# Kernel tuning notes

Hardware: AMD Instinct MI355X
Metric: run time of the kernel (lower is better)

## Reference

```python
import jax, jax.numpy as jnp
import numpy as np

B, LI, LC = 2, 1024, 256
H, NH, HD = 1024, 16, 64
MLP = 4096
EPS = 1e-6


def rmsnorm(x, w):
    return x * jax.lax.rsqrt(jnp.mean(x * x, axis=-1, keepdims=True) + EPS) * w


def apply_rope(x, cos, sin):
    # x: [B, NH, S, HD]; cos/sin: [S, HD]; rotate-half convention
    x1, x2 = jnp.split(x, 2, axis=-1)
    rot = jnp.concatenate([-x2, x1], axis=-1)
    return x * cos + rot * sin


def project_qkv(x, w, b):
    # x: [B, S, H] -> q,k,v each [B, NH, S, HD]
    bsz, s, _ = x.shape
    qkv = (x @ w.T + b).reshape(bsz, s, 3, NH, HD)
    qkv = jnp.transpose(qkv, (2, 0, 3, 1, 4))
    return qkv[0], qkv[1], qkv[2]


def setup_inputs() -> dict:
    key = jax.random.key(0)
    ks = iter(jax.random.split(key, 40))
    n = lambda shape, scale=1.0: jax.random.normal(next(ks), shape, dtype=jnp.float32) * scale
    xav = lambda fo, fi: n((fo, fi), float(np.sqrt(2.0 / (fo + fi))))
    inp = {
        'image_tokens': n((B, LI, H)),
        'condition_tokens': n((B, LC, H)),
        'image_rope_cos': n((LI, HD)),
        'image_rope_sin': n((LI, HD)),
        'cond_rope_cos': n((LC, HD)),
        'cond_rope_sin': n((LC, HD)),
        'img_norm1_w': jnp.ones((H,)), 'cond_norm1_w': jnp.ones((H,)),
        'img_qkv_w': xav(3 * H, H), 'img_qkv_b': jnp.zeros((3 * H,)),
        'cond_qkv_w': xav(3 * H, H), 'cond_qkv_b': jnp.zeros((3 * H,)),
        'img_qn_w': jnp.ones((HD,)), 'img_kn_w': jnp.ones((HD,)),
        'cond_qn_w': jnp.ones((HD,)), 'cond_kn_w': jnp.ones((HD,)),
        'img_out_w': xav(H, H), 'img_out_b': jnp.zeros((H,)),
        'cond_out_w': xav(H, H), 'cond_out_b': jnp.zeros((H,)),
        'img_norm2_w': jnp.ones((H,)), 'cond_norm2_w': jnp.ones((H,)),
        'img_mlp_w1': xav(MLP, H), 'img_mlp_b1': jnp.zeros((MLP,)),
        'img_mlp_w2': xav(MLP, H), 'img_mlp_b2': jnp.zeros((MLP,)),
        'img_mlp_w3': xav(H, MLP), 'img_mlp_b3': jnp.zeros((H,)),
        'cond_mlp_w1': xav(MLP, H), 'cond_mlp_b1': jnp.zeros((MLP,)),
        'cond_mlp_w2': xav(MLP, H), 'cond_mlp_b2': jnp.zeros((MLP,)),
        'cond_mlp_w3': xav(H, MLP), 'cond_mlp_b3': jnp.zeros((H,)),
        'alpha': jnp.zeros((1,)), 'beta': jnp.zeros((1,)),
    }
    return inp


def swiglu(x, w1, b1, w2, b2, w3, b3):
    return (jax.nn.silu(x @ w1.T + b1) * (x @ w2.T + b2)) @ w3.T + b3


def reference(image_tokens, condition_tokens, image_rope_cos, image_rope_sin,
              cond_rope_cos, cond_rope_sin, img_norm1_w, cond_norm1_w,
              img_qkv_w, img_qkv_b, cond_qkv_w, cond_qkv_b,
              img_qn_w, img_kn_w, cond_qn_w, cond_kn_w,
              img_out_w, img_out_b, cond_out_w, cond_out_b,
              img_norm2_w, cond_norm2_w,
              img_mlp_w1, img_mlp_b1, img_mlp_w2, img_mlp_b2, img_mlp_w3, img_mlp_b3,
              cond_mlp_w1, cond_mlp_b1, cond_mlp_w2, cond_mlp_b2, cond_mlp_w3, cond_mlp_b3,
              alpha, beta):
    img_res, cond_res = image_tokens, condition_tokens
    iq, ik, iv = project_qkv(rmsnorm(image_tokens, img_norm1_w), img_qkv_w, img_qkv_b)
    cq, ck, cv = project_qkv(rmsnorm(condition_tokens, cond_norm1_w), cond_qkv_w, cond_qkv_b)
    iq = apply_rope(rmsnorm(iq, img_qn_w), image_rope_cos, image_rope_sin)
    ik = apply_rope(rmsnorm(ik, img_kn_w), image_rope_cos, image_rope_sin)
    cq = apply_rope(rmsnorm(cq, cond_qn_w), cond_rope_cos, cond_rope_sin)
    ck = apply_rope(rmsnorm(ck, cond_kn_w), cond_rope_cos, cond_rope_sin)
    q = jnp.concatenate([cq, iq], axis=2)  # [B, NH, LC+LI, HD]
    k = jnp.concatenate([ck, ik], axis=2)
    v = jnp.concatenate([cv, iv], axis=2)
    scores = jnp.einsum('bhqd,bhkd->bhqk', q, k) / jnp.sqrt(jnp.float32(HD)).astype(q.dtype)
    attn = jax.nn.softmax(scores, axis=-1)
    out = jnp.einsum('bhqk,bhkd->bhqd', attn, v)
    cond_o, img_o = out[:, :, :LC], out[:, :, LC:]
    cond_o = jnp.transpose(cond_o, (0, 2, 1, 3)).reshape(B, LC, H)
    img_o = jnp.transpose(img_o, (0, 2, 1, 3)).reshape(B, LI, H)
    condition_tokens = cond_res + (cond_o @ cond_out_w.T + cond_out_b)
    image_tokens = img_res + alpha.reshape(1, 1, 1) * (img_o @ img_out_w.T + img_out_b)
    condition_tokens = condition_tokens + swiglu(rmsnorm(condition_tokens, cond_norm2_w),
                                                 cond_mlp_w1, cond_mlp_b1, cond_mlp_w2, cond_mlp_b2, cond_mlp_w3, cond_mlp_b3)
    image_tokens = image_tokens + beta.reshape(1, 1, 1) * swiglu(rmsnorm(image_tokens, img_norm2_w),
                                                                 img_mlp_w1, img_mlp_b1, img_mlp_w2, img_mlp_b2, img_mlp_w3, img_mlp_b3)
    return image_tokens, condition_tokens
```

## Files before the change

kernel.cpp:

```cpp
#include <hip/hip_runtime.h>
#include <hip/hip_bf16.h>

#define BB   2
#define LI   1024
#define LC   256
#define SEQ  1280
#define HDIM 1024
#define NH   16
#define HD   64
#define MLPD 4096
#define EPS  1e-6f
#define MROWS 2560
#define MTI  16
#define MTT  20

typedef __bf16 bf16x8 __attribute__((ext_vector_type(8)));
typedef float f32x4 __attribute__((ext_vector_type(4)));
typedef unsigned short us4 __attribute__((ext_vector_type(4)));
typedef unsigned short us8 __attribute__((ext_vector_type(8)));

static __device__ __forceinline__ unsigned short f2bf(float f) {
    unsigned int u = __builtin_bit_cast(unsigned int, f);
    u += 0x7fffu + ((u >> 16) & 1u);
    return (unsigned short)(u >> 16);
}
static __device__ __forceinline__ float bf2f(unsigned short h) {
    unsigned int u = ((unsigned int)h) << 16;
    return __builtin_bit_cast(float, u);
}

static __device__ __forceinline__ void gload_lds16(const void* g, void* l) {
    __builtin_amdgcn_global_load_lds((__attribute__((address_space(1))) void*)(g),
                                     (__attribute__((address_space(3))) void*)(l),
                                     16, 0, 0);
}

__global__ __launch_bounds__(256)
void pack_weights(const float* __restrict__ w1i, const float* __restrict__ w2i,
                  const float* __restrict__ w1c, const float* __restrict__ w2c,
                  const float* __restrict__ w3i, const float* __restrict__ w3c,
                  const float* __restrict__ wqi, const float* __restrict__ wqc,
                  const float* __restrict__ woi, const float* __restrict__ woc,
                  unsigned short* __restrict__ wpi, unsigned short* __restrict__ wpc,
                  unsigned short* __restrict__ w3bi, unsigned short* __restrict__ w3bc,
                  unsigned short* __restrict__ wqbi, unsigned short* __restrict__ wqbc,
                  unsigned short* __restrict__ wobi, unsigned short* __restrict__ wobc)
{
    const int seg = blockIdx.y;
    const float* s0 = nullptr; const float* s1 = nullptr;
    unsigned short* dst = nullptr; int n4 = 0; bool pair = false;
    switch (seg) {
        case 0: pair = true; s0 = w1i; s1 = w2i; dst = wpi;  n4 = 8388608 / 4; break;
        case 1: pair = true; s0 = w1c; s1 = w2c; dst = wpc;  n4 = 8388608 / 4; break;
        case 2: s0 = w3i; dst = w3bi; n4 = 4194304 / 4; break;
        case 3: s0 = w3c; dst = w3bc; n4 = 4194304 / 4; break;
        case 4: s0 = wqi; dst = wqbi; n4 = 3145728 / 4; break;
        case 5: s0 = wqc; dst = wqbc; n4 = 3145728 / 4; break;
        case 6: s0 = woi; dst = wobi; n4 = 1048576 / 4; break;
        case 7: s0 = woc; dst = wobc; n4 = 1048576 / 4; break;
    }
    for (int i = blockIdx.x * 256 + threadIdx.x; i < n4; i += gridDim.x * 256) {
        float4 v;
        if (pair) {
            int p  = i >> 8;
            int k4 = i & 255;
            int g = p >> 4, r = p & 15;
            const float* s = (g & 1) ? s1 : s0;
            v = *(const float4*)&s[((size_t)((g >> 1) * 16 + r)) * 1024 + k4 * 4];
        } else {
            v = ((const float4*)s0)[i];
        }
        us4 o = { f2bf(v.x), f2bf(v.y), f2bf(v.z), f2bf(v.w) };
        ((us4*)dst)[i] = o;
    }
}

__global__ __launch_bounds__(256)
void rmsnorm1(const float* __restrict__ img, const float* __restrict__ cond,
              const float* __restrict__ wi, const float* __restrict__ wc,
              unsigned short* __restrict__ xn)
{
    const int row = blockIdx.x;
    const int t   = threadIdx.x;
    const float* x = (row < 2048) ? img + (size_t)row * HDIM
                                  : cond + (size_t)(row - 2048) * HDIM;
    const float* w = (row < 2048) ? wi : wc;
    float4 v = ((const float4*)x)[t];
    float ss = v.x*v.x + v.y*v.y + v.z*v.z + v.w*v.w;
    for (int o = 32; o > 0; o >>= 1) ss += __shfl_xor(ss, o);
    __shared__ float red[4];
    if ((t & 63) == 0) red[t >> 6] = ss;
    __syncthreads();
    float inv = rsqrtf((red[0]+red[1]+red[2]+red[3]) * (1.0f / HDIM) + EPS);
    float4 wv = ((const float4*)w)[t];
    us4 pk = { f2bf(v.x*inv*wv.x), f2bf(v.y*inv*wv.y),
               f2bf(v.z*inv*wv.z), f2bf(v.w*inv*wv.w) };
    *(us4*)&xn[(size_t)row * HDIM + t * 4] = pk;
}

__global__ __launch_bounds__(256)
void rmsnorm2(const float* __restrict__ img_tok, const float* __restrict__ cond_tok,
              const float* __restrict__ op, const float* __restrict__ wi,
              const float* __restrict__ wc, const float* __restrict__ alpha,
              unsigned short* __restrict__ n2)
{
    const int row = blockIdx.x;
    const int t   = threadIdx.x;
    const bool img = row < 2048;
    const float sc = img ? alpha[0] : 1.0f;
    const float* tok = img ? img_tok + (size_t)row * HDIM
                           : cond_tok + (size_t)(row - 2048) * HDIM;
    const float* w = img ? wi : wc;
    float4 tv = ((const float4*)tok)[t];
    float4 ov = ((const float4*)(op + (size_t)row * HDIM))[t];
    float4 v = { tv.x + sc*ov.x, tv.y + sc*ov.y, tv.z + sc*ov.z, tv.w + sc*ov.w };
    float ss = v.x*v.x + v.y*v.y + v.z*v.z + v.w*v.w;
    for (int o = 32; o > 0; o >>= 1) ss += __shfl_xor(ss, o);
    __shared__ float red[4];
    if ((t & 63) == 0) red[t >> 6] = ss;
    __syncthreads();
    float inv = rsqrtf((red[0]+red[1]+red[2]+red[3]) * (1.0f / HDIM) + EPS);
    float4 wv = ((const float4*)w)[t];
    us4 pk = { f2bf(v.x*inv*wv.x), f2bf(v.y*inv*wv.y),
               f2bf(v.z*inv*wv.z), f2bf(v.w*inv*wv.w) };
    *(us4*)&n2[(size_t)row * HDIM + t * 4] = pk;
}

__global__ __launch_bounds__(256)
void op_init(const float* __restrict__ bi, const float* __restrict__ bc,
             float* __restrict__ op)
{
    const int row = blockIdx.x, t = threadIdx.x;
    const float* b = (row < 2048) ? bi : bc;
    ((float4*)(op + (size_t)row * HDIM))[t] = ((const float4*)b)[t];
}

__global__ __launch_bounds__(256)
void down_init(const float* __restrict__ img_tok, const float* __restrict__ cond_tok,
               const float* __restrict__ op, const float* __restrict__ b3i,
               const float* __restrict__ b3c, const float* __restrict__ alpha,
               const float* __restrict__ beta, float* __restrict__ out)
{
    const int row = blockIdx.x, t = threadIdx.x;
    const bool img = row < 2048;
    const float sa = img ? alpha[0] : 1.0f;
    const float sm = img ? beta[0]  : 1.0f;
    const float* tok = img ? img_tok + (size_t)row * HDIM
                           : cond_tok + (size_t)(row - 2048) * HDIM;
    const float* b3 = img ? b3i : b3c;
    float4 tv = ((const float4*)tok)[t];
    float4 ov = ((const float4*)(op + (size_t)row * HDIM))[t];
    float4 bv = ((const float4*)b3)[t];
    float4 o4 = { tv.x + sa*ov.x + sm*bv.x, tv.y + sa*ov.y + sm*bv.y,
                  tv.z + sa*ov.z + sm*bv.z, tv.w + sa*ov.w + sm*bv.w };
    ((float4*)(out + (size_t)row * HDIM))[t] = o4;
}

__global__ __launch_bounds__(256)
void qkv_gemm(const unsigned short* __restrict__ xn,
              const unsigned short* __restrict__ wqi, const unsigned short* __restrict__ wqc,
              const float* __restrict__ bi, const float* __restrict__ bc,
              unsigned short* __restrict__ qh, unsigned short* __restrict__ kh,
              unsigned short* __restrict__ vt)
{
    __shared__ __align__(16) unsigned short As[128][32];
    __shared__ __align__(16) unsigned short Ws[128][32];

    const int id  = blockIdx.x;
    const int xcd = id & 7, idx = id >> 3;
    const int xcol = xcd * 3 + idx / 20;
    const int mt   = idx % 20;
    const bool img = mt < MTI;
    const int row0 = img ? mt * 128 : 2048 + (mt - MTI) * 128;
    const int grow0 = img ? mt * 128 : (mt - MTI) * 128;
    const unsigned short* W = img ? wqi : wqc;
    const float* bias = img ? bi : bc;
    const int bn = xcol * 128;

    const int t = threadIdx.x, lane = t & 63, wid = t >> 6;
    const int wm = wid >> 1, wn = wid & 1;
    const int srow = (wid << 5) + (lane >> 2);
    const int scol = (lane & 3) << 3;
    const unsigned short* Ag0 = xn + (size_t)(row0 + srow)      * HDIM + scol;
    const unsigned short* Ag1 = xn + (size_t)(row0 + srow + 16) * HDIM + scol;
    const unsigned short* Wg0 = W  + (size_t)(bn + srow)        * HDIM + scol;
    const unsigned short* Wg1 = W  + (size_t)(bn + srow + 16)   * HDIM + scol;
    unsigned short* lA0 = &As[(wid << 5)     ][0];
    unsigned short* lA1 = &As[(wid << 5) + 16][0];
    unsigned short* lW0 = &Ws[(wid << 5)     ][0];
    unsigned short* lW1 = &Ws[(wid << 5) + 16][0];

    const int fr = lane & 15, kg = lane >> 4, ko = kg << 3;
    f32x4 acc[4][4] = {};

    for (int k0 = 0; k0 < HDIM; k0 += 32) {
        __syncthreads();
        gload_lds16(Ag0 + k0, lA0);
        gload_lds16(Ag1 + k0, lA1);
        gload_lds16(Wg0 + k0, lW0);
        gload_lds16(Wg1 + k0, lW1);
        __syncthreads();
        bf16x8 aF[4], bF[4];
#pragma unroll
        for (int m = 0; m < 4; ++m) aF[m] = *(const bf16x8*)&As[wm*64 + m*16 + fr][ko];
#pragma unroll
        for (int n = 0; n < 4; ++n) bF[n] = *(const bf16x8*)&Ws[wn*64 + n*16 + fr][ko];
#pragma unroll
        for (int m = 0; m < 4; ++m)
#pragma unroll
            for (int n = 0; n < 4; ++n)
                acc[m][n] = __builtin_amdgcn_mfma_f32_16x16x32_bf16(aF[m], bF[n], acc[m][n], 0,0,0);
    }

#pragma unroll
    for (int n = 0; n < 4; ++n) {
        const int gc = bn + wn*64 + n*16 + fr;
        const int which = gc >> 10;
        const int h = (gc >> 6) & 15, d = gc & 63;
        const float bv = bias[gc];
#pragma unroll
        for (int m = 0; m < 4; ++m) {
            const int gl0 = grow0 + wm*64 + m*16 + (kg << 2);
            int b, s0;
            if (img) { b = gl0 >> 10; s0 = LC + (gl0 & 1023); }
            else     { b = gl0 >> 8;  s0 = gl0 & 255; }
            if (which == 2) {
                us4 pk = { f2bf(acc[m][n][0] + bv), f2bf(acc[m][n][1] + bv),
                           f2bf(acc[m][n][2] + bv), f2bf(acc[m][n][3] + bv) };
                *(us4*)&vt[(((size_t)(b*NH + h)) * HD + d) * SEQ + s0] = pk;
            } else {
                unsigned short* dst = (which == 0) ? qh : kh;
#pragma unroll
                for (int j = 0; j < 4; ++j)
                    dst[(((size_t)(b*NH + h)) * SEQ + s0 + j) * HD + d] = f2bf(acc[m][n][j] + bv);
            }
        }
    }
}

__global__ __launch_bounds__(256)
void pair_gemm(const unsigned short* __restrict__ n2,
               const unsigned short* __restrict__ wpi, const unsigned short* __restrict__ wpc,
               const float* __restrict__ b1i, const float* __restrict__ b2i,
               const float* __restrict__ b1c, const float* __restrict__ b2c,
               unsigned short* __restrict__ hbf)
{
    __shared__ __align__(16) unsigned short As[128][64];
    __shared__ __align__(16) unsigned short Ws[128][64];

    const int id  = blockIdx.x;
    const int xcd = id & 7, idx = id >> 3;
    const int x   = xcd * 8 + idx / 20;
    const int mt  = idx % 20;
    const bool img = mt < MTI;
    const int row0 = img ? mt * 128 : 2048 + (mt - MTI) * 128;
    const unsigned short* W = img ? wpi : wpc;
    const float* b1 = img ? b1i : b1c;
    const float* b2 = img ? b2i : b2c;
    const int bn = x * 128;

    const int t = threadIdx.x, lane = t & 63, wid = t >> 6;
    const int wm = wid >> 1, wn = wid & 1;
    const int fr = lane & 15, kg = lane >> 4;

    const int ch_r[4] = { ((wid*4+0)*64 + lane) >> 3, ((wid*4+1)*64 + lane) >> 3,
                          ((wid*4+2)*64 + lane) >> 3, ((wid*4+3)*64 + lane) >> 3 };
    const int ch_c[4] = { (((wid*4+0)*64 + lane) & 7) ^ (ch_r[0] & 7),
                          (((wid*4+1)*64 + lane) & 7) ^ (ch_r[1] & 7),
                          (((wid*4+2)*64 + lane) & 7) ^ (ch_r[2] & 7),
                          (((wid*4+3)*64 + lane) & 7) ^ (ch_r[3] & 7) };

    f32x4 acc[4][4] = {};

    for (int k0 = 0; k0 < HDIM; k0 += 64) {
        __syncthreads();
#pragma unroll
        for (int i = 0; i < 4; ++i) {
            gload_lds16(n2 + (size_t)(row0 + ch_r[i]) * HDIM + k0 + ch_c[i]*8,
                        &As[0][0] + (size_t)(wid*4 + i) * 64 * 8);
            gload_lds16(W  + (size_t)(bn   + ch_r[i]) * HDIM + k0 + ch_c[i]*8,
                        &Ws[0][0] + (size_t)(wid*4 + i) * 64 * 8);
        }
        __syncthreads();
#pragma unroll
        for (int kc = 0; kc < 2; ++kc) {
            bf16x8 aF[4], bF[4];
#pragma unroll
            for (int m = 0; m < 4; ++m) {
                const int r = wm*64 + m*16 + fr;
                aF[m] = *(const bf16x8*)&As[r][(((kc*4 + kg) ^ (r & 7)) << 3)];
            }
#pragma unroll
            for (int n = 0; n < 4; ++n) {
                const int r = wn*64 + n*16 + fr;
                bF[n] = *(const bf16x8*)&Ws[r][(((kc*4 + kg) ^ (r & 7)) << 3)];
            }
#pragma unroll
            for (int m = 0; m < 4; ++m)
#pragma unroll
                for (int n = 0; n < 4; ++n)
                    acc[m][n] = __builtin_amdgcn_mfma_f32_16x16x32_bf16(aF[m], bF[n], acc[m][n], 0,0,0);
        }
    }

#pragma unroll
    for (int p = 0; p < 2; ++p) {
        const int lc = (4*x + 2*wn + p) * 16 + fr;
        const float b1v = b1[lc], b2v = b2[lc];
#pragma unroll
        for (int m = 0; m < 4; ++m) {
#pragma unroll
            for (int j = 0; j < 4; ++j) {
                const int row = row0 + wm*64 + m*16 + (kg << 2) + j;
                float g1 = acc[m][2*p    ][j] + b1v;
                float g2 = acc[m][2*p + 1][j] + b2v;
                float hv = (g1 / (1.0f + __expf(-g1))) * g2;
                hbf[(size_t)row * MLPD + lc] = f2bf(hv);
            }
        }
    }
}

__global__ __launch_bounds__(256)
void skg_gemm(const unsigned short* __restrict__ A, int K,
              const unsigned short* __restrict__ Wimg, const unsigned short* __restrict__ Wcond,
              float* __restrict__ out, int kchunk,
              const float* __restrict__ sci, const float* __restrict__ scc)
{
    __shared__ __align__(16) unsigned short As[128][32];
    __shared__ __align__(16) unsigned short Ws[128][32];

    const int id  = blockIdx.x;
    const int xcd = id & 7, idx = id >> 3;
    const int bn  = xcd * 128;
    const int mt  = idx % 20;
    const int kz  = idx / 20;
    const bool img = mt < MTI;
    const int row0 = img ? mt * 128 : 2048 + (mt - MTI) * 128;
    const unsigned short* W = img ? Wimg : Wcond;
    const float sc = img ? (sci ? sci[0] : 1.0f) : (scc ? scc[0] : 1.0f);
    const int kbase = kz * kchunk;

    const int t = threadIdx.x, lane = t & 63, wid = t >> 6;
    const int wm = wid >> 1, wn = wid & 1;
    const int srow = (wid << 5) + (lane >> 2);
    const int scol = (lane & 3) << 3;
    const unsigned short* Ag0 = A + (size_t)(row0 + srow)      * K + kbase + scol;
    const unsigned short* Ag1 = A + (size_t)(row0 + srow + 16) * K + kbase + scol;
    const unsigned short* Wg0 = W + (size_t)(bn + srow)        * K + kbase + scol;
    const unsigned short* Wg1 = W + (size_t)(bn + srow + 16)   * K + kbase + scol;
    unsigned short* lA0 = &As[(wid << 5)     ][0];
    unsigned short* lA1 = &As[(wid << 5) + 16][0];
    unsigned short* lW0 = &Ws[(wid << 5)     ][0];
    unsigned short* lW1 = &Ws[(wid << 5) + 16][0];

    const int fr = lane & 15, kg = lane >> 4, ko = kg << 3;
    f32x4 acc[4][4] = {};

    for (int k0 = 0; k0 < kchunk; k0 += 32) {
        __syncthreads();
        gload_lds16(Ag0 + k0, lA0);
        gload_lds16(Ag1 + k0, lA1);
        gload_lds16(Wg0 + k0, lW0);
        gload_lds16(Wg1 + k0, lW1);
        __syncthreads();
        bf16x8 aF[4], bF[4];
#pragma unroll
        for (int m = 0; m < 4; ++m) aF[m] = *(const bf16x8*)&As[wm*64 + m*16 + fr][ko];
#pragma unroll
        for (int n = 0; n < 4; ++n) bF[n] = *(const bf16x8*)&Ws[wn*64 + n*16 + fr][ko];
#pragma unroll
        for (int m = 0; m < 4; ++m)
#pragma unroll
            for (int n = 0; n < 4; ++n)
                acc[m][n] = __builtin_amdgcn_mfma_f32_16x16x32_bf16(aF[m], bF[n], acc[m][n], 0,0,0);
    }

#pragma unroll
    for (int n = 0; n < 4; ++n) {
        const int col = bn + wn*64 + n*16 + fr;
#pragma unroll
        for (int m = 0; m < 4; ++m) {
            const int r0 = row0 + wm*64 + m*16 + (kg << 2);
#pragma unroll
            for (int j = 0; j < 4; ++j)
                unsafeAtomicAdd(&out[(size_t)(r0 + j) * HDIM + col], sc * acc[m][n][j]);
        }
    }
}

__launch_bounds__(256)
__global__ void qkv_prep(unsigned short* __restrict__ qh, unsigned short* __restrict__ kh,
                         const float* __restrict__ img_qn, const float* __restrict__ img_kn,
                         const float* __restrict__ cond_qn, const float* __restrict__ cond_kn,
                         const float* __restrict__ icos, const float* __restrict__ isin,
                         const float* __restrict__ ccos, const float* __restrict__ csin)
{
    const int L = blockIdx.x * 4 + (threadIdx.x >> 6);
    const int d = threadIdx.x & 63;
    const int b = L / (NH * SEQ);
    const int rem = L - b * NH * SEQ;
    const int h = rem / SEQ;
    const int s = rem - h * SEQ;

    const float *qw, *kw, *cs, *sn;
    if (s < LC) { qw = cond_qn; kw = cond_kn;
                  cs = ccos + (size_t)s * HD; sn = csin + (size_t)s * HD; }
    else        { qw = img_qn; kw = img_kn;
                  cs = icos + (size_t)(s - LC) * HD; sn = isin + (size_t)(s - LC) * HD; }
    const size_t idx = (((size_t)(b*NH + h)) * SEQ + s) * HD + d;
    float qv = bf2f(qh[idx]);
    float kv = bf2f(kh[idx]);

    float sq = qv * qv;
    for (int o = 32; o > 0; o >>= 1) sq += __shfl_xor(sq, o);
    float qn = qv * rsqrtf(sq * (1.0f / HD) + EPS) * qw[d];
    float sk = kv * kv;
    for (int o = 32; o > 0; o >>= 1) sk += __shfl_xor(sk, o);
    float kn = kv * rsqrtf(sk * (1.0f / HD) + EPS) * kw[d];

    const float c = cs[d], s_ = sn[d];
    float qp = __shfl_xor(qn, 32);
    float kp = __shfl_xor(kn, 32);
    float qrot = (d < 32) ? -qp : qp;
    float krot = (d < 32) ? -kp : kp;
    qh[idx] = f2bf((qn * c + qrot * s_) * 0.125f);
    kh[idx] = f2bf(kn * c + krot * s_);
}

__global__ __launch_bounds__(256)
void attn_mfma(const unsigned short* __restrict__ qg,
               const unsigned short* __restrict__ kg,
               const unsigned short* __restrict__ vtg,
               unsigned short* __restrict__ o)
{
    const int id  = blockIdx.x;
    const int xcd = id & 7, idx = id >> 3;
    const int bh  = xcd * 4 + idx / 10;
    const int q0  = (idx % 10) * 128;
    const int h   = bh & 15;
    const int b   = bh >> 4;
    const int t   = threadIdx.x;
    const int wid = t >> 6;
    const int lane = t & 63;
    const int g  = lane >> 4;
    const int fr = lane & 15;

    __shared__ __align__(16) unsigned short Ks [2][64 * 64];
    __shared__ __align__(16) unsigned short VTs[2][64 * 64];
    __shared__ __align__(16) unsigned short Ps [4][32][72];

    const unsigned short* qb  = qg  + (size_t)bh * SEQ * HD;
    const unsigned short* kb  = kg  + (size_t)bh * SEQ * HD;
    const unsigned short* vtb = vtg + (size_t)bh * HD * SEQ;

    bf16x8 Qf[2][2];
#pragma unroll
    for (int mt = 0; mt < 2; ++mt)
#pragma unroll
        for (int kc = 0; kc < 2; ++kc)
            Qf[mt][kc] = *(const bf16x8*)&qb[(size_t)(q0 + wid*32 + mt*16 + fr) * HD
                                             + kc*32 + g*8];

    f32x4 O[2][4] = {};
    float mreg[2] = { -3e38f, -3e38f };
    float lreg[2] = { 0.f, 0.f };

#define STAGE(tile_, bufi_)                                                     \
    {                                                                           \
        _Pragma("unroll")                                                       \
        for (int i = 0; i < 2; ++i) {                                           \
            int chbase = i * 256 + wid * 64;                                    \
            int ch = chbase + lane;                                             \
            int r = ch >> 3, c = ch & 7;                                        \
            int cs_ = c ^ (r & 7);                                              \
            gload_lds16(kb  + (size_t)((tile_)*64 + r) * HD + cs_*8,            \
                        &Ks[bufi_][chbase * 8]);                                \
            gload_lds16(vtb + (size_t)r * SEQ + (tile_)*64 + cs_*8,             \
                        &VTs[bufi_][chbase * 8]);                               \
        }                                                                       \
    }

    STAGE(0, 0);
    __syncthreads();
    int buf = 0;

    for (int tile = 0; tile < SEQ / 64; ++tile) {
        if (tile + 1 < SEQ / 64) STAGE(tile + 1, buf ^ 1);

        f32x4 ST[2][4] = {};
#pragma unroll
        for (int kc = 0; kc < 2; ++kc)
#pragma unroll
            for (int nt = 0; nt < 4; ++nt) {
                int r = fr + 16*nt;
                bf16x8 kf = *(const bf16x8*)&Ks[buf][r*64 + (((g + 4*kc) ^ (r & 7)) * 8)];
#pragma unroll
                for (int mt = 0; mt < 2; ++mt)
                    ST[mt][nt] = __builtin_amdgcn_mfma_f32_16x16x32_bf16(
                        kf, Qf[mt][kc], ST[mt][nt], 0, 0, 0);
            }

#pragma unroll
        for (int mt = 0; mt < 2; ++mt) {
            float tm = -3e38f;
#pragma unroll
            for (int nt = 0; nt < 4; ++nt)
#pragma unroll
                for (int j = 0; j < 4; ++j) tm = fmaxf(tm, ST[mt][nt][j]);
            tm = fmaxf(tm, __shfl_xor(tm, 16));
            tm = fmaxf(tm, __shfl_xor(tm, 32));
            float mn = fmaxf(mreg[mt], tm);
            float al = __expf(mreg[mt] - mn);
            mreg[mt] = mn;
            float ls = 0.f;
#pragma unroll
            for (int nt = 0; nt < 4; ++nt) {
#pragma unroll
                for (int j = 0; j < 4; ++j) {
                    float p = __expf(ST[mt][nt][j] - mn);
                    ST[mt][nt][j] = p;
                    ls += p;
                }
            }
            ls += __shfl_xor(ls, 16);
            ls += __shfl_xor(ls, 32);
            lreg[mt] = al * lreg[mt] + ls;
            f32x4 alr;
#pragma unroll
            for (int rg = 0; rg < 4; ++rg) alr[rg] = __shfl(al, 4*g + rg);
#pragma unroll
            for (int dt = 0; dt < 4; ++dt) O[mt][dt] *= alr;
#pragma unroll
            for (int nt = 0; nt < 4; ++nt) {
                us4 pk = { f2bf(ST[mt][nt][0]), f2bf(ST[mt][nt][1]),
                           f2bf(ST[mt][nt][2]), f2bf(ST[mt][nt][3]) };
                *(us4*)&Ps[wid][mt*16 + fr][16*nt + 4*g] = pk;
            }
        }

#pragma unroll
        for (int kc = 0; kc < 2; ++kc) {
            bf16x8 Pf[2];
#pragma unroll
            for (int mt = 0; mt < 2; ++mt)
                Pf[mt] = *(const bf16x8*)&Ps[wid][mt*16 + fr][kc*32 + g*8];
#pragma unroll
            for (int dt = 0; dt < 4; ++dt) {
                int r = fr + 16*dt;
                bf16x8 vf = *(const bf16x8*)&VTs[buf][r*64 + (((g + 4*kc) ^ (r & 7)) * 8)];
#pragma unroll
                for (int mt = 0; mt < 2; ++mt)
                    O[mt][dt] = __builtin_amdgcn_mfma_f32_16x16x32_bf16(
                        Pf[mt], vf, O[mt][dt], 0, 0, 0);
            }
        }

        __syncthreads();
        buf ^= 1;
    }

#pragma unroll
    for (int mt = 0; mt < 2; ++mt) {
        const float linv = 1.0f / lreg[mt];
        f32x4 lv;
#pragma unroll
        for (int rg = 0; rg < 4; ++rg) lv[rg] = __shfl(linv, 4*g + rg);
#pragma unroll
        for (int rg = 0; rg < 4; ++rg) {
            const int s_tok = q0 + wid*32 + mt*16 + 4*g + rg;
            const size_t row = (s_tok < LC) ? (size_t)(2048 + b*LC + s_tok)
                                            : (size_t)(b*LI + (s_tok - LC));
#pragma unroll
            for (int dt = 0; dt < 4; ++dt)
                o[row * HDIM + h*HD + 16*dt + fr] = f2bf(O[mt][dt][rg] * lv[rg]);
        }
    }
#undef STAGE
}

extern "C" void kernel_launch(void* const* d_in, const int* in_sizes, int n_in,
                              void* d_out, int out_size, void* d_ws, size_t ws_size,
                              hipStream_t stream)
{
    const float* image_tokens = (const float*)d_in[0];
    const float* cond_tokens  = (const float*)d_in[1];
    const float* icos  = (const float*)d_in[2];
    const float* isin  = (const float*)d_in[3];
    const float* ccos  = (const float*)d_in[4];
    const float* csin  = (const float*)d_in[5];
    const float* img_n1w  = (const float*)d_in[6];
    const float* cond_n1w = (const float*)d_in[7];
    const float* img_qkv_w  = (const float*)d_in[8];
    const float* img_qkv_b  = (const float*)d_in[9];
    const float* cond_qkv_w = (const float*)d_in[10];
    const float* cond_qkv_b = (const float*)d_in[11];
    const float* img_qn  = (const float*)d_in[12];
    const float* img_kn  = (const float*)d_in[13];
    const float* cond_qn = (const float*)d_in[14];
    const float* cond_kn = (const float*)d_in[15];
    const float* img_out_w  = (const float*)d_in[16];
    const float* img_out_b  = (const float*)d_in[17];
    const float* cond_out_w = (const float*)d_in[18];
    const float* cond_out_b = (const float*)d_in[19];
    const float* img_n2w  = (const float*)d_in[20];
    const float* cond_n2w = (const float*)d_in[21];
    const float* img_w1 = (const float*)d_in[22];
    const float* img_b1 = (const float*)d_in[23];
    const float* img_w2 = (const float*)d_in[24];
    const float* img_b2 = (const float*)d_in[25];
    const float* img_w3 = (const float*)d_in[26];
    const float* img_b3 = (const float*)d_in[27];
    const float* cond_w1 = (const float*)d_in[28];
    const float* cond_b1 = (const float*)d_in[29];
    const float* cond_w2 = (const float*)d_in[30];
    const float* cond_b2 = (const float*)d_in[31];
    const float* cond_w3 = (const float*)d_in[32];
    const float* cond_b3 = (const float*)d_in[33];
    const float* alpha = (const float*)d_in[34];
    const float* beta  = (const float*)d_in[35];

    float* out = (float*)d_out;

    unsigned short* u = (unsigned short*)d_ws;
    unsigned short* wp_i  = u + 0;
    unsigned short* wp_c  = u + 8388608;
    unsigned short* w3b_i = u + 16777216;
    unsigned short* w3b_c = u + 20971520;
    unsigned short* wqb_i = u + 25165824;
    unsigned short* wqb_c = u + 28311552;
    unsigned short* wob_i = u + 31457280;
    unsigned short* wob_c = u + 32505856;
    unsigned short* xn = u + 33554432;
    unsigned short* vt = u + 36175872;
    unsigned short* qh = u + 38797312;
    unsigned short* kh = u + 41418752;
    unsigned short* o  = u + 44040192;
    float*          op = (float*)(u + 38797312);
    unsigned short* n2 = u + 36175872;
    unsigned short* hbf = u + 25165824;

    pack_weights<<<dim3(512, 8), 256, 0, stream>>>(
        img_w1, img_w2, cond_w1, cond_w2, img_w3, cond_w3,
        img_qkv_w, cond_qkv_w, img_out_w, cond_out_w,
        wp_i, wp_c, w3b_i, w3b_c, wqb_i, wqb_c, wob_i, wob_c);

    rmsnorm1<<<MROWS, 256, 0, stream>>>(image_tokens, cond_tokens, img_n1w, cond_n1w, xn);

    qkv_gemm<<<480, 256, 0, stream>>>(
        xn, wqb_i, wqb_c, img_qkv_b, cond_qkv_b, qh, kh, vt);

    qkv_prep<<<BB * NH * SEQ / 4, 256, 0, stream>>>(
        qh, kh, img_qn, img_kn, cond_qn, cond_kn, icos, isin, ccos, csin);

    attn_mfma<<<320, 256, 0, stream>>>(qh, kh, vt, o);

    op_init<<<MROWS, 256, 0, stream>>>(img_out_b, cond_out_b, op);
    skg_gemm<<<8 * MTT * 2, 256, 0, stream>>>(
        o, HDIM, wob_i, wob_c, op, HDIM / 2, nullptr, nullptr);

    rmsnorm2<<<MROWS, 256, 0, stream>>>(
        image_tokens, cond_tokens, op, img_n2w, cond_n2w, alpha, n2);

    pair_gemm<<<1280, 256, 0, stream>>>(
        n2, wp_i, wp_c, img_b1, img_b2, cond_b1, cond_b2, hbf);

    down_init<<<MROWS, 256, 0, stream>>>(
        image_tokens, cond_tokens, op, img_b3, cond_b3, alpha, beta, out);
    skg_gemm<<<8 * MTT * 4, 256, 0, stream>>>(
        hbf, MLPD, w3b_i, w3b_c, out, MLPD / 4, beta, nullptr);
}
```

Baseline: 296.2 us.

## Fuse norms, RoPE and init kernels into neighbours; shrink pair_gemm K tile

Moves rmsnorm1 into extra blocks of the weight-pack kernel and fuses the QK-norm and RoPE epilogue into the QKV GEMM, which removes the qkv_prep kernel and its read-modify-write of q and k. It also merges rmsnorm2 with down_init so the residual and bias init are written in one pass. Separately, pair_gemm drops from a swizzled 64-wide K tile to an unswizzled 32-wide tile. That halves LDS use but doubles the barrier count and may bring back LDS bank conflicts. The fused QKV epilogue writes q and k with scattered 2-byte stores and reads the cos/sin tables per element.

```diff
diff --git a/kernel.cpp b/kernel.cpp
--- a/kernel.cpp
+++ b/kernel.cpp
@@ -17,16 +17,11 @@
 typedef __bf16 bf16x8 __attribute__((ext_vector_type(8)));
 typedef float f32x4 __attribute__((ext_vector_type(4)));
 typedef unsigned short us4 __attribute__((ext_vector_type(4)));
-typedef unsigned short us8 __attribute__((ext_vector_type(8)));
 
 static __device__ __forceinline__ unsigned short f2bf(float f) {
     unsigned int u = __builtin_bit_cast(unsigned int, f);
     u += 0x7fffu + ((u >> 16) & 1u);
     return (unsigned short)(u >> 16);
-}
-static __device__ __forceinline__ float bf2f(unsigned short h) {
-    unsigned int u = ((unsigned int)h) << 16;
-    return __builtin_bit_cast(float, u);
 }
 
 static __device__ __forceinline__ void gload_lds16(const void* g, void* l) {
@@ -44,9 +39,37 @@
                   unsigned short* __restrict__ wpi, unsigned short* __restrict__ wpc,
                   unsigned short* __restrict__ w3bi, unsigned short* __restrict__ w3bc,
                   unsigned short* __restrict__ wqbi, unsigned short* __restrict__ wqbc,
-                  unsigned short* __restrict__ wobi, unsigned short* __restrict__ wobc)
+                  unsigned short* __restrict__ wobi, unsigned short* __restrict__ wobc,
+                  const float* __restrict__ img_tok, const float* __restrict__ cond_tok,
+                  const float* __restrict__ n1wi, const float* __restrict__ n1wc,
+                  unsigned short* __restrict__ xn)
 {
     const int seg = blockIdx.y;
+    const int t = threadIdx.x;
+
+    if (seg == 8) {
+        __shared__ float red[4];
+#pragma unroll
+        for (int rr = 0; rr < 4; ++rr) {
+            const int row = blockIdx.x * 4 + rr;
+            const float* x = (row < 2048) ? img_tok + (size_t)row * HDIM
+                                          : cond_tok + (size_t)(row - 2048) * HDIM;
+            const float* w = (row < 2048) ? n1wi : n1wc;
+            float4 v = ((const float4*)x)[t];
+            float ss = v.x*v.x + v.y*v.y + v.z*v.z + v.w*v.w;
+            for (int o = 32; o > 0; o >>= 1) ss += __shfl_xor(ss, o);
+            if ((t & 63) == 0) red[t >> 6] = ss;
+            __syncthreads();
+            float inv = rsqrtf((red[0]+red[1]+red[2]+red[3]) * (1.0f / HDIM) + EPS);
+            float4 wv = ((const float4*)w)[t];
+            us4 pk = { f2bf(v.x*inv*wv.x), f2bf(v.y*inv*wv.y),
+                       f2bf(v.z*inv*wv.z), f2bf(v.w*inv*wv.w) };
+            *(us4*)&xn[(size_t)row * HDIM + t * 4] = pk;
+            __syncthreads();
+        }
+        return;
+    }
+
     const float* s0 = nullptr; const float* s1 = nullptr;
     unsigned short* dst = nullptr; int n4 = 0; bool pair = false;
     switch (seg) {
@@ -59,7 +82,7 @@
         case 6: s0 = woi; dst = wobi; n4 = 1048576 / 4; break;
         case 7: s0 = woc; dst = wobc; n4 = 1048576 / 4; break;
     }
-    for (int i = blockIdx.x * 256 + threadIdx.x; i < n4; i += gridDim.x * 256) {
+    for (int i = blockIdx.x * 256 + t; i < n4; i += gridDim.x * 256) {
         float4 v;
         if (pair) {
             int p  = i >> 8;
@@ -76,44 +99,25 @@
 }
 
 __global__ __launch_bounds__(256)
-void rmsnorm1(const float* __restrict__ img, const float* __restrict__ cond,
-              const float* __restrict__ wi, const float* __restrict__ wc,
-              unsigned short* __restrict__ xn)
-{
-    const int row = blockIdx.x;
-    const int t   = threadIdx.x;
-    const float* x = (row < 2048) ? img + (size_t)row * HDIM
-                                  : cond + (size_t)(row - 2048) * HDIM;
-    const float* w = (row < 2048) ? wi : wc;
-    float4 v = ((const float4*)x)[t];
-    float ss = v.x*v.x + v.y*v.y + v.z*v.z + v.w*v.w;
-    for (int o = 32; o > 0; o >>= 1) ss += __shfl_xor(ss, o);
-    __shared__ float red[4];
-    if ((t & 63) == 0) red[t >> 6] = ss;
-    __syncthreads();
-    float inv = rsqrtf((red[0]+red[1]+red[2]+red[3]) * (1.0f / HDIM) + EPS);
-    float4 wv = ((const float4*)w)[t];
-    us4 pk = { f2bf(v.x*inv*wv.x), f2bf(v.y*inv*wv.y),
-               f2bf(v.z*inv*wv.z), f2bf(v.w*inv*wv.w) };
-    *(us4*)&xn[(size_t)row * HDIM + t * 4] = pk;
-}
-
-__global__ __launch_bounds__(256)
-void rmsnorm2(const float* __restrict__ img_tok, const float* __restrict__ cond_tok,
-              const float* __restrict__ op, const float* __restrict__ wi,
-              const float* __restrict__ wc, const float* __restrict__ alpha,
-              unsigned short* __restrict__ n2)
+void norm2_down(const float* __restrict__ img_tok, const float* __restrict__ cond_tok,
+                const float* __restrict__ op, const float* __restrict__ wi,
+                const float* __restrict__ wc, const float* __restrict__ b3i,
+                const float* __restrict__ b3c, const float* __restrict__ alpha,
+                const float* __restrict__ beta,
+                unsigned short* __restrict__ n2, float* __restrict__ out)
 {
     const int row = blockIdx.x;
     const int t   = threadIdx.x;
     const bool img = row < 2048;
-    const float sc = img ? alpha[0] : 1.0f;
+    const float sa = img ? alpha[0] : 1.0f;
+    const float sm = img ? beta[0]  : 1.0f;
     const float* tok = img ? img_tok + (size_t)row * HDIM
                            : cond_tok + (size_t)(row - 2048) * HDIM;
-    const float* w = img ? wi : wc;
+    const float* w  = img ? wi  : wc;
+    const float* b3 = img ? b3i : b3c;
     float4 tv = ((const float4*)tok)[t];
     float4 ov = ((const float4*)(op + (size_t)row * HDIM))[t];
-    float4 v = { tv.x + sc*ov.x, tv.y + sc*ov.y, tv.z + sc*ov.z, tv.w + sc*ov.w };
+    float4 v = { tv.x + sa*ov.x, tv.y + sa*ov.y, tv.z + sa*ov.z, tv.w + sa*ov.w };
     float ss = v.x*v.x + v.y*v.y + v.z*v.z + v.w*v.w;
     for (int o = 32; o > 0; o >>= 1) ss += __shfl_xor(ss, o);
     __shared__ float red[4];
@@ -124,6 +128,9 @@
     us4 pk = { f2bf(v.x*inv*wv.x), f2bf(v.y*inv*wv.y),
                f2bf(v.z*inv*wv.z), f2bf(v.w*inv*wv.w) };
     *(us4*)&n2[(size_t)row * HDIM + t * 4] = pk;
+    float4 bv = ((const float4*)b3)[t];
+    float4 o4 = { v.x + sm*bv.x, v.y + sm*bv.y, v.z + sm*bv.z, v.w + sm*bv.w };
+    ((float4*)(out + (size_t)row * HDIM))[t] = o4;
 }
 
 __global__ __launch_bounds__(256)
@@ -133,33 +140,16 @@
     const int row = blockIdx.x, t = threadIdx.x;
     const float* b = (row < 2048) ? bi : bc;
     ((float4*)(op + (size_t)row * HDIM))[t] = ((const float4*)b)[t];
-}
-
-__global__ __launch_bounds__(256)
-void down_init(const float* __restrict__ img_tok, const float* __restrict__ cond_tok,
-               const float* __restrict__ op, const float* __restrict__ b3i,
-               const float* __restrict__ b3c, const float* __restrict__ alpha,
-               const float* __restrict__ beta, float* __restrict__ out)
-{
-    const int row = blockIdx.x, t = threadIdx.x;
-    const bool img = row < 2048;
-    const float sa = img ? alpha[0] : 1.0f;
-    const float sm = img ? beta[0]  : 1.0f;
-    const float* tok = img ? img_tok + (size_t)row * HDIM
-                           : cond_tok + (size_t)(row - 2048) * HDIM;
-    const float* b3 = img ? b3i : b3c;
-    float4 tv = ((const float4*)tok)[t];
-    float4 ov = ((const float4*)(op + (size_t)row * HDIM))[t];
-    float4 bv = ((const float4*)b3)[t];
-    float4 o4 = { tv.x + sa*ov.x + sm*bv.x, tv.y + sa*ov.y + sm*bv.y,
-                  tv.z + sa*ov.z + sm*bv.z, tv.w + sa*ov.w + sm*bv.w };
-    ((float4*)(out + (size_t)row * HDIM))[t] = o4;
 }
 
 __global__ __launch_bounds__(256)
 void qkv_gemm(const unsigned short* __restrict__ xn,
               const unsigned short* __restrict__ wqi, const unsigned short* __restrict__ wqc,
               const float* __restrict__ bi, const float* __restrict__ bc,
+              const float* __restrict__ img_qn, const float* __restrict__ img_kn,
+              const float* __restrict__ cond_qn, const float* __restrict__ cond_kn,
+              const float* __restrict__ icos, const float* __restrict__ isin,
+              const float* __restrict__ ccos, const float* __restrict__ csin,
               unsigned short* __restrict__ qh, unsigned short* __restrict__ kh,
               unsigned short* __restrict__ vt)
 {
@@ -212,27 +202,71 @@
                 acc[m][n] = __builtin_amdgcn_mfma_f32_16x16x32_bf16(aF[m], bF[n], acc[m][n], 0,0,0);
     }
 
-#pragma unroll
-    for (int n = 0; n < 4; ++n) {
-        const int gc = bn + wn*64 + n*16 + fr;
-        const int which = gc >> 10;
-        const int h = (gc >> 6) & 15, d = gc & 63;
-        const float bv = bias[gc];
-#pragma unroll
-        for (int m = 0; m < 4; ++m) {
-            const int gl0 = grow0 + wm*64 + m*16 + (kg << 2);
-            int b, s0;
-            if (img) { b = gl0 >> 10; s0 = LC + (gl0 & 1023); }
-            else     { b = gl0 >> 8;  s0 = gl0 & 255; }
-            if (which == 2) {
+    const int gcbase = bn + wn * 64;
+    const int which  = gcbase >> 10;
+    const int h      = (gcbase >> 6) & 15;
+
+    if (which == 2) {
+#pragma unroll
+        for (int n = 0; n < 4; ++n) {
+            const int d = n*16 + fr;
+            const float bv = bias[gcbase + d];
+#pragma unroll
+            for (int m = 0; m < 4; ++m) {
+                const int gl0 = grow0 + wm*64 + m*16 + (kg << 2);
+                int b, s0;
+                if (img) { b = gl0 >> 10; s0 = LC + (gl0 & 1023); }
+                else     { b = gl0 >> 8;  s0 = gl0 & 255; }
                 us4 pk = { f2bf(acc[m][n][0] + bv), f2bf(acc[m][n][1] + bv),
                            f2bf(acc[m][n][2] + bv), f2bf(acc[m][n][3] + bv) };
                 *(us4*)&vt[(((size_t)(b*NH + h)) * HD + d) * SEQ + s0] = pk;
-            } else {
-                unsigned short* dst = (which == 0) ? qh : kh;
-#pragma unroll
-                for (int j = 0; j < 4; ++j)
-                    dst[(((size_t)(b*NH + h)) * SEQ + s0 + j) * HD + d] = f2bf(acc[m][n][j] + bv);
+            }
+        }
+    } else {
+        unsigned short* dst = (which == 0) ? qh : kh;
+        const float qscale = (which == 0) ? 0.125f : 1.0f;
+        const float* nw = img ? (which == 0 ? img_qn : img_kn)
+                              : (which == 0 ? cond_qn : cond_kn);
+        const float* cs_tab = img ? icos : ccos;
+        const float* sn_tab = img ? isin : csin;
+        float wv[4], bv[4];
+#pragma unroll
+        for (int nt = 0; nt < 4; ++nt) {
+            wv[nt] = nw[nt*16 + fr];
+            bv[nt] = bias[gcbase + nt*16 + fr];
+        }
+#pragma unroll
+        for (int m = 0; m < 4; ++m) {
+#pragma unroll
+            for (int j = 0; j < 4; ++j) {
+                const int gl = grow0 + wm*64 + m*16 + (kg << 2) + j;
+                int b, srel, s;
+                if (img) { b = gl >> 10; srel = gl & 1023; s = LC + srel; }
+                else     { b = gl >> 8;  srel = gl & 255;  s = srel; }
+                float v[4];
+                float ss = 0.f;
+#pragma unroll
+                for (int nt = 0; nt < 4; ++nt) {
+                    v[nt] = acc[m][nt][j] + bv[nt];
+                    ss += v[nt] * v[nt];
+                }
+                ss += __shfl_xor(ss, 1);
+                ss += __shfl_xor(ss, 2);
+                ss += __shfl_xor(ss, 4);
+                ss += __shfl_xor(ss, 8);
+                const float inv = rsqrtf(ss * (1.0f / HD) + EPS);
+                float xv[4];
+#pragma unroll
+                for (int nt = 0; nt < 4; ++nt) xv[nt] = v[nt] * inv * wv[nt];
+                const size_t obase = (((size_t)(b*NH + h)) * SEQ + s) * HD;
+#pragma unroll
+                for (int nt = 0; nt < 4; ++nt) {
+                    const int d = nt*16 + fr;
+                    const float rot = (nt < 2) ? -xv[nt + 2] : xv[nt - 2];
+                    const float c  = cs_tab[(size_t)srel * HD + d];
+                    const float sn = sn_tab[(size_t)srel * HD + d];
+                    dst[obase + d] = f2bf((xv[nt] * c + rot * sn) * qscale);
+                }
             }
         }
     }
@@ -245,8 +279,8 @@
                const float* __restrict__ b1c, const float* __restrict__ b2c,
                unsigned short* __restrict__ hbf)
 {
-    __shared__ __align__(16) unsigned short As[128][64];
-    __shared__ __align__(16) unsigned short Ws[128][64];
+    __shared__ __align__(16) unsigned short As[128][32];
+    __shared__ __align__(16) unsigned short Ws[128][32];
 
     const int id  = blockIdx.x;
     const int xcd = id & 7, idx = id >> 3;
@@ -261,46 +295,37 @@
 
     const int t = threadIdx.x, lane = t & 63, wid = t >> 6;
     const int wm = wid >> 1, wn = wid & 1;
-    const int fr = lane & 15, kg = lane >> 4;
-
-    const int ch_r[4] = { ((wid*4+0)*64 + lane) >> 3, ((wid*4+1)*64 + lane) >> 3,
-                          ((wid*4+2)*64 + lane) >> 3, ((wid*4+3)*64 + lane) >> 3 };
-    const int ch_c[4] = { (((wid*4+0)*64 + lane) & 7) ^ (ch_r[0] & 7),
-                          (((wid*4+1)*64 + lane) & 7) ^ (ch_r[1] & 7),
-                          (((wid*4+2)*64 + lane) & 7) ^ (ch_r[2] & 7),
-                          (((wid*4+3)*64 + lane) & 7) ^ (ch_r[3] & 7) };
-
+    const int srow = (wid << 5) + (lane >> 2);
+    const int scol = (lane & 3) << 3;
+    const unsigned short* Ag0 = n2 + (size_t)(row0 + srow)      * HDIM + scol;
+    const unsigned short* Ag1 = n2 + (size_t)(row0 + srow + 16) * HDIM + scol;
+    const unsigned short* Wg0 = W  + (size_t)(bn + srow)        * HDIM + scol;
+    const unsigned short* Wg1 = W  + (size_t)(bn + srow + 16)   * HDIM + scol;
+    unsigned short* lA0 = &As[(wid << 5)     ][0];
+    unsigned short* lA1 = &As[(wid << 5) + 16][0];
+    unsigned short* lW0 = &Ws[(wid << 5)     ][0];
+    unsigned short* lW1 = &Ws[(wid << 5) + 16][0];
+
+    const int fr = lane & 15, kg = lane >> 4, ko = kg << 3;
     f32x4 acc[4][4] = {};
 
-    for (int k0 = 0; k0 < HDIM; k0 += 64) {
+    for (int k0 = 0; k0 < HDIM; k0 += 32) {
         __syncthreads();
-#pragma unroll
-        for (int i = 0; i < 4; ++i) {
-            gload_lds16(n2 + (size_t)(row0 + ch_r[i]) * HDIM + k0 + ch_c[i]*8,
-                        &As[0][0] + (size_t)(wid*4 + i) * 64 * 8);
-            gload_lds16(W  + (size_t)(bn   + ch_r[i]) * HDIM + k0 + ch_c[i]*8,
-                        &Ws[0][0] + (size_t)(wid*4 + i) * 64 * 8);
-        }
+        gload_lds16(Ag0 + k0, lA0);
+        gload_lds16(Ag1 + k0, lA1);
+        gload_lds16(Wg0 + k0, lW0);
+        gload_lds16(Wg1 + k0, lW1);
         __syncthreads();
-#pragma unroll
-        for (int kc = 0; kc < 2; ++kc) {
-            bf16x8 aF[4], bF[4];
-#pragma unroll
-            for (int m = 0; m < 4; ++m) {
-                const int r = wm*64 + m*16 + fr;
-                aF[m] = *(const bf16x8*)&As[r][(((kc*4 + kg) ^ (r & 7)) << 3)];
-            }
-#pragma unroll
-            for (int n = 0; n < 4; ++n) {
-                const int r = wn*64 + n*16 + fr;
-                bF[n] = *(const bf16x8*)&Ws[r][(((kc*4 + kg) ^ (r & 7)) << 3)];
-            }
-#pragma unroll
-            for (int m = 0; m < 4; ++m)
-#pragma unroll
-                for (int n = 0; n < 4; ++n)
-                    acc[m][n] = __builtin_amdgcn_mfma_f32_16x16x32_bf16(aF[m], bF[n], acc[m][n], 0,0,0);
-        }
+        bf16x8 aF[4], bF[4];
+#pragma unroll
+        for (int m = 0; m < 4; ++m) aF[m] = *(const bf16x8*)&As[wm*64 + m*16 + fr][ko];
+#pragma unroll
+        for (int n = 0; n < 4; ++n) bF[n] = *(const bf16x8*)&Ws[wn*64 + n*16 + fr][ko];
+#pragma unroll
+        for (int m = 0; m < 4; ++m)
+#pragma unroll
+            for (int n = 0; n < 4; ++n)
+                acc[m][n] = __builtin_amdgcn_mfma_f32_16x16x32_bf16(aF[m], bF[n], acc[m][n], 0,0,0);
     }
 
 #pragma unroll
@@ -387,45 +412,6 @@
                 unsafeAtomicAdd(&out[(size_t)(r0 + j) * HDIM + col], sc * acc[m][n][j]);
         }
     }
-}
-
-__launch_bounds__(256)
-__global__ void qkv_prep(unsigned short* __restrict__ qh, unsigned short* __restrict__ kh,
-                         const float* __restrict__ img_qn, const float* __restrict__ img_kn,
-                         const float* __restrict__ cond_qn, const float* __restrict__ cond_kn,
-                         const float* __restrict__ icos, const float* __restrict__ isin,
-                         const float* __restrict__ ccos, const float* __restrict__ csin)
-{
-    const int L = blockIdx.x * 4 + (threadIdx.x >> 6);
-    const int d = threadIdx.x & 63;
-    const int b = L / (NH * SEQ);
-    const int rem = L - b * NH * SEQ;
-    const int h = rem / SEQ;
-    const int s = rem - h * SEQ;
-
-    const float *qw, *kw, *cs, *sn;
-    if (s < LC) { qw = cond_qn; kw = cond_kn;
-                  cs = ccos + (size_t)s * HD; sn = csin + (size_t)s * HD; }
-    else        { qw = img_qn; kw = img_kn;
-                  cs = icos + (size_t)(s - LC) * HD; sn = isin + (size_t)(s - LC) * HD; }
-    const size_t idx = (((size_t)(b*NH + h)) * SEQ + s) * HD + d;
-    float qv = bf2f(qh[idx]);
-    float kv = bf2f(kh[idx]);
-
-    float sq = qv * qv;
-    for (int o = 32; o > 0; o >>= 1) sq += __shfl_xor(sq, o);
-    float qn = qv * rsqrtf(sq * (1.0f / HD) + EPS) * qw[d];
-    float sk = kv * kv;
-    for (int o = 32; o > 0; o >>= 1) sk += __shfl_xor(sk, o);
-    float kn = kv * rsqrtf(sk * (1.0f / HD) + EPS) * kw[d];
-
-    const float c = cs[d], s_ = sn[d];
-    float qp = __shfl_xor(qn, 32);
-    float kp = __shfl_xor(kn, 32);
-    float qrot = (d < 32) ? -qp : qp;
-    float krot = (d < 32) ? -kp : kp;
-    qh[idx] = f2bf((qn * c + qrot * s_) * 0.125f);
-    kh[idx] = f2bf(kn * c + krot * s_);
 }
 
 __global__ __launch_bounds__(256)
@@ -640,18 +626,16 @@
     unsigned short* n2 = u + 36175872;
     unsigned short* hbf = u + 25165824;
 
-    pack_weights<<<dim3(512, 8), 256, 0, stream>>>(
+    pack_weights<<<dim3(640, 9), 256, 0, stream>>>(
         img_w1, img_w2, cond_w1, cond_w2, img_w3, cond_w3,
         img_qkv_w, cond_qkv_w, img_out_w, cond_out_w,
-        wp_i, wp_c, w3b_i, w3b_c, wqb_i, wqb_c, wob_i, wob_c);
-
-    rmsnorm1<<<MROWS, 256, 0, stream>>>(image_tokens, cond_tokens, img_n1w, cond_n1w, xn);
+        wp_i, wp_c, w3b_i, w3b_c, wqb_i, wqb_c, wob_i, wob_c,
+        image_tokens, cond_tokens, img_n1w, cond_n1w, xn);
 
     qkv_gemm<<<480, 256, 0, stream>>>(
-        xn, wqb_i, wqb_c, img_qkv_b, cond_qkv_b, qh, kh, vt);
-
-    qkv_prep<<<BB * NH * SEQ / 4, 256, 0, stream>>>(
-        qh, kh, img_qn, img_kn, cond_qn, cond_kn, icos, isin, ccos, csin);
+        xn, wqb_i, wqb_c, img_qkv_b, cond_qkv_b,
+        img_qn, img_kn, cond_qn, cond_kn, icos, isin, ccos, csin,
+        qh, kh, vt);
 
     attn_mfma<<<320, 256, 0, stream>>>(qh, kh, vt, o);
 
@@ -659,14 +643,13 @@
     skg_gemm<<<8 * MTT * 2, 256, 0, stream>>>(
         o, HDIM, wob_i, wob_c, op, HDIM / 2, nullptr, nullptr);
 
-    rmsnorm2<<<MROWS, 256, 0, stream>>>(
-        image_tokens, cond_tokens, op, img_n2w, cond_n2w, alpha, n2);
+    norm2_down<<<MROWS, 256, 0, stream>>>(
+        image_tokens, cond_tokens, op, img_n2w, cond_n2w,
+        img_b3, cond_b3, alpha, beta, n2, out);
 
     pair_gemm<<<1280, 256, 0, stream>>>(
         n2, wp_i, wp_c, img_b1, img_b2, cond_b1, cond_b2, hbf);
 
-    down_init<<<MROWS, 256, 0, stream>>>(
-        image_tokens, cond_tokens, op, img_b3, cond_b3, alpha, beta, out);
     skg_gemm<<<8 * MTT * 4, 256, 0, stream>>>(
         hbf, MLPD, w3b_i, w3b_c, out, MLPD / 4, beta, nullptr);
 }
```

After: 293.1 us. Within noise of the previous version (-1.1%).
